# Optimization experiments

Hardware: AMD Instinct MI355X
Metric: run time of the kernel (lower is better)

## Reference

```python
import math
import jax, jax.numpy as jnp
import numpy as np

N = 50000          # nodes
E = 1_600_000      # edges
DNE = 128
DED = 128
NUM_RBF = 50
R_CUT = 5.0
LN_EPS = 1e-5


def setup_inputs() -> dict:
    key = jax.random.key(0)
    ks = jax.random.split(key, 16)
    z = jax.random.normal(ks[0], (N, 25), jnp.float32)
    edge = jax.random.randint(ks[1], (E, 2), 0, N, dtype=jnp.int64)
    r = jax.random.uniform(ks[2], (E,), jnp.float32) * (R_CUT * 1.1)  # some beyond cutoff
    u_raw = jax.random.normal(ks[3], (E, 3), jnp.float32)
    u = u_raw / jnp.linalg.norm(u_raw, axis=-1, keepdims=True)

    def xavier(k, shape):
        fan_in, fan_out = shape
        lim = math.sqrt(6.0 / (fan_in + fan_out))
        return jax.random.uniform(k, shape, jnp.float32, -lim, lim)

    return {
        "z": z, "edge": edge, "r": r, "u": u,
        "A_na_w": xavier(ks[4], (25, DNE)), "A_na_b": jnp.zeros((DNE,), jnp.float32),
        "A_nbr_w": xavier(ks[5], (25, DNE)), "A_nbr_b": jnp.zeros((DNE,), jnp.float32),
        "W_ndp_w": xavier(ks[6], (NUM_RBF, DNE)), "W_ndp_b": jnp.zeros((DNE,), jnp.float32),
        "W_nrd_w": xavier(ks[7], (2 * DNE, DNE)), "W_nrd_b": jnp.zeros((DNE,), jnp.float32),
        "W_nru_w": xavier(ks[8], (DNE, DNE)), "W_nru_b": jnp.zeros((DNE,), jnp.float32),
        "W_erp_w": xavier(ks[9], (NUM_RBF, DED)), "W_erp_b": jnp.zeros((DED,), jnp.float32),
        "ln_g": jnp.ones((DNE,), jnp.float32), "ln_b": jnp.zeros((DNE,), jnp.float32),
    }


def _sh_l2(u):
    x, y, zc = u[:, 0], u[:, 1], u[:, 2]
    s3 = math.sqrt(3.0)
    return jnp.stack([
        s3 * x * y,
        s3 * y * zc,
        0.5 * (3.0 * zc * zc - 1.0),
        s3 * zc * x,
        0.5 * s3 * (x * x - y * y),
    ], axis=-1)  # [E, 5]


def _rbf(r):
    start = math.exp(-R_CUT)
    means = jnp.linspace(start, 1.0, NUM_RBF)
    beta = (2.0 / NUM_RBF * (1.0 - start)) ** (-2)
    alpha = 5.0 / R_CUT
    return jnp.exp(-beta * (jnp.exp(-alpha * r[:, None]) - means) ** 2)  # [E, NUM_RBF]


def reference(z, edge, r, u,
              A_na_w, A_na_b, A_nbr_w, A_nbr_b,
              W_ndp_w, W_ndp_b, W_nrd_w, W_nrd_b,
              W_nru_w, W_nru_b, W_erp_w, W_erp_b,
              ln_g, ln_b):
    i, j = edge[:, 0], edge[:, 1]
    n_nodes = z.shape[0]

    # edge tensor representations (Lmax=2)
    rt0 = r[:, None]          # [E,1]
    rt1 = u                   # [E,3]
    rt2 = _sh_l2(u)           # [E,5]

    rbf = _rbf(r)                                              # [E,R]
    c = (0.5 * (jnp.cos(math.pi * r / R_CUT) + 1.0)
         * (r < R_CUT).astype(r.dtype))[:, None]               # [E,1]

    nbr = jax.nn.silu(z @ A_nbr_w + A_nbr_b)                   # [N,dne]
    gate = (rbf @ W_ndp_w + W_ndp_b) * c                       # [E,dne]
    msg = nbr[j] * gate                                        # gather + gate
    m = jax.ops.segment_sum(msg, i, num_segments=n_nodes)      # scatter-add [N,dne]

    na = jax.nn.silu(z @ A_na_w + A_na_b)
    h = jnp.concatenate([na, m], axis=-1) @ W_nrd_w + W_nrd_b  # [N,dne]
    mu = jnp.mean(h, axis=-1, keepdims=True)
    var = jnp.var(h, axis=-1, keepdims=True)
    h = (h - mu) / jnp.sqrt(var + LN_EPS) * ln_g + ln_b
    h = jax.nn.silu(h)
    h = h @ W_nru_w + W_nru_b                                  # [N,dne]

    t = (h[i] + h[j]) * (rbf @ W_erp_w + W_erp_b)              # [E,ded]
    return (h, t, rt0, rt1, rt2, c)
```

## Files before the change

kernel.cpp:

```cpp
#include <hip/hip_runtime.h>
#include <hip/hip_bf16.h>
#include <math.h>

#define NN 50000
#define NE 1600000
#define D 128
#define NRBF 50
#define RCUT 5.0f
#define LNEPS 1e-5f
#define EB 16
#define EB2 64
#define EDGE_GRID 2048
#define SCAN_B 196
#define NB 16
#define NPB 8

typedef __attribute__((ext_vector_type(8))) short bf16x8;
typedef __attribute__((ext_vector_type(4))) float f32x4;

__device__ __forceinline__ float silu_f(float x) {
    return x / (1.0f + __expf(-x));
}
__device__ __forceinline__ unsigned short f2bf(float x) {
    __hip_bfloat16 b = __float2bfloat16(x);
    return *reinterpret_cast<unsigned short*>(&b);
}
__device__ __forceinline__ float bf2f(unsigned short u) {
    unsigned int x = ((unsigned int)u) << 16;
    return __uint_as_float(x);
}

__global__ __launch_bounds__(128) void nbr_kernel(
    const float* __restrict__ z, const float* __restrict__ Aw,
    const float* __restrict__ Ab, unsigned short* __restrict__ nbr_bf)
{
    const int n = blockIdx.x;
    const int d = threadIdx.x;
    float acc = Ab[d];
#pragma unroll
    for (int k = 0; k < 25; ++k)
        acc = fmaf(z[n * 25 + k], Aw[k * D + d], acc);
    nbr_bf[(size_t)n * D + d] = f2bf(silu_f(acc));
}

__global__ __launch_bounds__(256) void aux_kernel(
    const int* __restrict__ edge, const float* __restrict__ r,
    const float* __restrict__ u, float* __restrict__ rt0,
    float* __restrict__ rt1, float* __restrict__ rt2,
    float* __restrict__ cout, int* __restrict__ cnt)
{
    const int e = blockIdx.x * 256 + threadIdx.x;
    if (e >= NE) return;
    const float rr = r[e];
    rt0[e] = rr;
    const float cc = (rr < RCUT)
        ? 0.5f * (__cosf(3.14159265358979f * rr * (1.0f / RCUT)) + 1.0f)
        : 0.0f;
    cout[e] = cc;
    const float x  = u[e * 3 + 0];
    const float y  = u[e * 3 + 1];
    const float zc = u[e * 3 + 2];
    rt1[(size_t)e * 3 + 0] = x;
    rt1[(size_t)e * 3 + 1] = y;
    rt1[(size_t)e * 3 + 2] = zc;
    const float s3 = 1.7320508075688772f;
    rt2[(size_t)e * 5 + 0] = s3 * x * y;
    rt2[(size_t)e * 5 + 1] = s3 * y * zc;
    rt2[(size_t)e * 5 + 2] = 0.5f * (3.0f * zc * zc - 1.0f);
    rt2[(size_t)e * 5 + 3] = s3 * zc * x;
    rt2[(size_t)e * 5 + 4] = 0.5f * s3 * (x * x - y * y);
    atomicAdd(&cnt[edge[2 * e]], 1);
}

__global__ __launch_bounds__(256) void scan1_kernel(
    const int* __restrict__ cnt, int* __restrict__ off, int* __restrict__ bsum)
{
    __shared__ int s[2][256];
    const int t = threadIdx.x;
    const int g = blockIdx.x * 256 + t;
    const int v = (g < NN) ? cnt[g] : 0;
    int incl = v;
    s[0][t] = incl;
    __syncthreads();
    int cur = 0;
#pragma unroll
    for (int dd = 1; dd < 256; dd <<= 1) {
        const int add = (t >= dd) ? s[cur][t - dd] : 0;
        incl += add;
        s[cur ^ 1][t] = incl;
        __syncthreads();
        cur ^= 1;
    }
    if (g < NN) off[g] = incl - v;
    if (t == 255) bsum[blockIdx.x] = incl;
}

__global__ __launch_bounds__(256) void scan2_kernel(int* __restrict__ bsum)
{
    __shared__ int s[2][256];
    const int t = threadIdx.x;
    const int v = (t < SCAN_B) ? bsum[t] : 0;
    int incl = v;
    s[0][t] = incl;
    __syncthreads();
    int cur = 0;
#pragma unroll
    for (int dd = 1; dd < 256; dd <<= 1) {
        const int add = (t >= dd) ? s[cur][t - dd] : 0;
        incl += add;
        s[cur ^ 1][t] = incl;
        __syncthreads();
        cur ^= 1;
    }
    if (t < SCAN_B) bsum[t] = incl - v;
}

__global__ __launch_bounds__(256) void scan3_kernel(
    int* __restrict__ off, const int* __restrict__ bsum)
{
    const int g = blockIdx.x * 256 + threadIdx.x;
    if (g < NN) off[g] += bsum[blockIdx.x];
    if (g == 0) off[NN] = NE;
}

__global__ __launch_bounds__(256) void scatter_kernel(
    const int* __restrict__ edge, const float* __restrict__ r,
    const int* __restrict__ off, int* __restrict__ cursor,
    uint2* __restrict__ jr)
{
    const int e = blockIdx.x * 256 + threadIdx.x;
    if (e >= NE) return;
    const int2 ep = ((const int2*)edge)[e];
    const int pos = atomicAdd(&cursor[ep.x], 1);
    uint2 v;
    v.x = (unsigned int)ep.y;
    v.y = __float_as_uint(r[e]);
    jr[off[ep.x] + pos] = v;
}

__global__ __launch_bounds__(128) void gather_msg_mfma(
    const uint2* __restrict__ jr, const int* __restrict__ off,
    const float* __restrict__ W_ndp, const float* __restrict__ b_ndp,
    const unsigned short* __restrict__ nbr_bf, float* __restrict__ m)
{
    __shared__ unsigned short P[EB][64];
    __shared__ float er_s[EB];
    __shared__ float c_s[EB];
    __shared__ int   j_s[EB];

    const int tid = threadIdx.x;
    const int w   = tid >> 6;
    const int l   = tid & 63;
    const int lr  = l & 15;
    const int lg  = l >> 4;

    bf16x8 wf[4][2];
#pragma unroll
    for (int dt = 0; dt < 4; ++dt) {
        const int col = w * 64 + lr * 4 + dt;
#pragma unroll
        for (int s = 0; s < 2; ++s) {
            bf16x8 v;
#pragma unroll
            for (int j = 0; j < 8; ++j) {
                const int k = s * 32 + lg * 8 + j;
                float wv = 0.0f;
                if (k < NRBF)       wv = W_ndp[k * D + col];
                else if (k == NRBF) wv = b_ndp[col];
                v[j] = (short)f2bf(wv);
            }
            wf[dt][s] = v;
        }
    }

    const float start = expf(-RCUT);
    const float step  = (1.0f - start) / (NRBF - 1);
    const float bq    = (2.0f / NRBF) * (1.0f - start);
    const float beta  = 1.0f / (bq * bq);

    const int prow = tid >> 3;
    const int pci  = tid & 7;

    for (int nn = 0; nn < NPB; ++nn) {
        const int n   = blockIdx.x * NPB + nn;
        const int s0  = off[n];
        const int deg = off[n + 1] - s0;

        f32x4 macc[4] = {{0,0,0,0},{0,0,0,0},{0,0,0,0},{0,0,0,0}};

        for (int base = 0; base < deg; base += EB) {
            const int chunk = min(EB, deg - base);
            if (tid < EB) {
                if (tid < chunk) {
                    const uint2 v = jr[s0 + base + tid];
                    const float rr = __uint_as_float(v.y);
                    er_s[tid] = __expf(-rr);
                    c_s[tid] = (rr < RCUT)
                        ? 0.5f * (__cosf(3.14159265358979f * rr * (1.0f / RCUT)) + 1.0f)
                        : 0.0f;
                    j_s[tid] = (int)v.x;
                } else {
                    er_s[tid] = 0.0f; c_s[tid] = 0.0f; j_s[tid] = 0;
                }
            }
            __syncthreads();
            {
                const float er = er_s[prow];
                const float cc = c_s[prow];
                unsigned int pk[4];
#pragma unroll
                for (int p2 = 0; p2 < 4; ++p2) {
                    unsigned int word = 0;
#pragma unroll
                    for (int c = 0; c < 2; ++c) {
                        const int k = pci * 8 + p2 * 2 + c;
                        float v = 0.0f;
                        if (k < NRBF) {
                            const float diff = er - (start + (float)k * step);
                            v = cc * __expf(-beta * diff * diff);
                        } else if (k == NRBF) {
                            v = cc;
                        }
                        word |= ((unsigned int)f2bf(v)) << (16 * c);
                    }
                    pk[p2] = word;
                }
                const int swc = pci ^ (prow & 7);
                *(uint4*)&P[prow][swc * 8] = make_uint4(pk[0], pk[1], pk[2], pk[3]);
            }
            __syncthreads();
            bf16x8 af[2];
#pragma unroll
            for (int s = 0; s < 2; ++s) {
                const int swc = (s * 4 + lg) ^ (lr & 7);
                af[s] = *(const bf16x8*)&P[lr][swc * 8];
            }
            f32x4 accs[4];
#pragma unroll
            for (int dt = 0; dt < 4; ++dt) {
                f32x4 acc = {0.0f, 0.0f, 0.0f, 0.0f};
                acc = __builtin_amdgcn_mfma_f32_16x16x32_bf16(af[0], wf[dt][0], acc, 0, 0, 0);
                acc = __builtin_amdgcn_mfma_f32_16x16x32_bf16(af[1], wf[dt][1], acc, 0, 0, 0);
                accs[dt] = acc;
            }
#pragma unroll
            for (int q = 0; q < 4; ++q) {
                const int row = j_s[lg * 4 + q];
                const uint2 nv8 = *(const uint2*)(nbr_bf + (size_t)row * D + w * 64 + lr * 4);
                const float n0 = bf2f((unsigned short)(nv8.x & 0xffff));
                const float n1 = bf2f((unsigned short)(nv8.x >> 16));
                const float n2 = bf2f((unsigned short)(nv8.y & 0xffff));
                const float n3 = bf2f((unsigned short)(nv8.y >> 16));
                macc[0][q] = fmaf(n0, accs[0][q], macc[0][q]);
                macc[1][q] = fmaf(n1, accs[1][q], macc[1][q]);
                macc[2][q] = fmaf(n2, accs[2][q], macc[2][q]);
                macc[3][q] = fmaf(n3, accs[3][q], macc[3][q]);
            }
            __syncthreads();
        }

        float v0 = macc[0][0] + macc[0][1] + macc[0][2] + macc[0][3];
        float v1 = macc[1][0] + macc[1][1] + macc[1][2] + macc[1][3];
        float v2 = macc[2][0] + macc[2][1] + macc[2][2] + macc[2][3];
        float v3 = macc[3][0] + macc[3][1] + macc[3][2] + macc[3][3];
        v0 += __shfl_xor(v0, 16); v0 += __shfl_xor(v0, 32);
        v1 += __shfl_xor(v1, 16); v1 += __shfl_xor(v1, 32);
        v2 += __shfl_xor(v2, 16); v2 += __shfl_xor(v2, 32);
        v3 += __shfl_xor(v3, 16); v3 += __shfl_xor(v3, 32);
        if (lg == 0) {
            float4 o = {v0, v1, v2, v3};
            *(float4*)&m[(size_t)n * D + w * 64 + lr * 4] = o;
        }
    }
}

__global__ __launch_bounds__(256) void node_kernel2(
    const float* __restrict__ z, const float* __restrict__ A_na_w,
    const float* __restrict__ A_na_b, const float* __restrict__ m,
    const float* __restrict__ W_nrd_w, const float* __restrict__ W_nrd_b,
    const float* __restrict__ W_nru_w, const float* __restrict__ W_nru_b,
    const float* __restrict__ ln_g, const float* __restrict__ ln_b,
    float* __restrict__ hout, unsigned short* __restrict__ h_bf)
{
    __shared__ float inbuf[NB][260];
    __shared__ float wbuf[32][128];
    __shared__ float part[4][NB][2];

    const int tid = threadIdx.x;
    const int n0 = blockIdx.x * NB;
    const int nl = tid & 15;
    const int dg = tid >> 4;

    for (int idx = tid; idx < NB * 128; idx += 256) {
        const int n = idx >> 7;
        const int d = idx & 127;
        float acc = A_na_b[d];
#pragma unroll
        for (int k = 0; k < 25; ++k)
            acc = fmaf(z[(size_t)(n0 + n) * 25 + k], A_na_w[k * D + d], acc);
        inbuf[n][d]       = silu_f(acc);
        inbuf[n][128 + d] = m[(size_t)(n0 + n) * D + d];
    }

    float h1[8];
#pragma unroll
    for (int dd = 0; dd < 8; ++dd) h1[dd] = W_nrd_b[dg * 8 + dd];

    for (int tile = 0; tile < 8; ++tile) {
        __syncthreads();
        for (int v = tid; v < 32 * 32; v += 256) {
            const int row = v >> 5;
            const int c4  = (v & 31) * 4;
            *(float4*)&wbuf[row][c4] =
                *(const float4*)&W_nrd_w[(size_t)(tile * 32 + row) * D + c4];
        }
        __syncthreads();
#pragma unroll 4
        for (int k = 0; k < 32; ++k) {
            const float rin = inbuf[nl][tile * 32 + k];
            const float4 wa = *(const float4*)&wbuf[k][dg * 8];
            const float4 wb = *(const float4*)&wbuf[k][dg * 8 + 4];
            h1[0] = fmaf(rin, wa.x, h1[0]);
            h1[1] = fmaf(rin, wa.y, h1[1]);
            h1[2] = fmaf(rin, wa.z, h1[2]);
            h1[3] = fmaf(rin, wa.w, h1[3]);
            h1[4] = fmaf(rin, wb.x, h1[4]);
            h1[5] = fmaf(rin, wb.y, h1[5]);
            h1[6] = fmaf(rin, wb.z, h1[6]);
            h1[7] = fmaf(rin, wb.w, h1[7]);
        }
    }

    float s = 0.0f, sq = 0.0f;
#pragma unroll
    for (int dd = 0; dd < 8; ++dd) { s += h1[dd]; sq += h1[dd] * h1[dd]; }
    s  += __shfl_xor(s, 16);  sq += __shfl_xor(sq, 16);
    s  += __shfl_xor(s, 32);  sq += __shfl_xor(sq, 32);
    const int wv = tid >> 6;
    if ((tid & 63) < 16) { part[wv][nl][0] = s; part[wv][nl][1] = sq; }
    __syncthreads();
    float ts = 0.0f, tsq = 0.0f;
#pragma unroll
    for (int w = 0; w < 4; ++w) { ts += part[w][nl][0]; tsq += part[w][nl][1]; }
    const float mu  = ts * (1.0f / 128.0f);
    const float var = tsq * (1.0f / 128.0f) - mu * mu;
    const float inv = rsqrtf(var + LNEPS);

#pragma unroll
    for (int dd = 0; dd < 8; ++dd) {
        const int d = dg * 8 + dd;
        inbuf[nl][d] = silu_f((h1[dd] - mu) * inv * ln_g[d] + ln_b[d]);
    }

    float h2[8];
#pragma unroll
    for (int dd = 0; dd < 8; ++dd) h2[dd] = W_nru_b[dg * 8 + dd];

    for (int tile = 0; tile < 4; ++tile) {
        __syncthreads();
        for (int v = tid; v < 32 * 32; v += 256) {
            const int row = v >> 5;
            const int c4  = (v & 31) * 4;
            *(float4*)&wbuf[row][c4] =
                *(const float4*)&W_nru_w[(size_t)(tile * 32 + row) * D + c4];
        }
        __syncthreads();
#pragma unroll 4
        for (int k = 0; k < 32; ++k) {
            const float rin = inbuf[nl][tile * 32 + k];
            const float4 wa = *(const float4*)&wbuf[k][dg * 8];
            const float4 wb = *(const float4*)&wbuf[k][dg * 8 + 4];
            h2[0] = fmaf(rin, wa.x, h2[0]);
            h2[1] = fmaf(rin, wa.y, h2[1]);
            h2[2] = fmaf(rin, wa.z, h2[2]);
            h2[3] = fmaf(rin, wa.w, h2[3]);
            h2[4] = fmaf(rin, wb.x, h2[4]);
            h2[5] = fmaf(rin, wb.y, h2[5]);
            h2[6] = fmaf(rin, wb.z, h2[6]);
            h2[7] = fmaf(rin, wb.w, h2[7]);
        }
    }

    float4 o0 = {h2[0], h2[1], h2[2], h2[3]};
    float4 o1 = {h2[4], h2[5], h2[6], h2[7]};
    *(float4*)&hout[(size_t)(n0 + nl) * D + dg * 8]     = o0;
    *(float4*)&hout[(size_t)(n0 + nl) * D + dg * 8 + 4] = o1;

    unsigned int b0 = (unsigned int)f2bf(h2[0]) | ((unsigned int)f2bf(h2[1]) << 16);
    unsigned int b1 = (unsigned int)f2bf(h2[2]) | ((unsigned int)f2bf(h2[3]) << 16);
    unsigned int b2 = (unsigned int)f2bf(h2[4]) | ((unsigned int)f2bf(h2[5]) << 16);
    unsigned int b3 = (unsigned int)f2bf(h2[6]) | ((unsigned int)f2bf(h2[7]) << 16);
    *(uint4*)&h_bf[(size_t)(n0 + nl) * D + dg * 8] = make_uint4(b0, b1, b2, b3);
}

__global__ __launch_bounds__(256) void edge_out_mfma(
    const int* __restrict__ edge, const float* __restrict__ r,
    const float* __restrict__ W_erp, const float* __restrict__ b_erp,
    const unsigned short* __restrict__ h_bf, float* __restrict__ t)
{
    __shared__ unsigned short P[EB2][64];
    __shared__ unsigned short hv[EB2][136];
    __shared__ int ij_s[EB2][2];

    const int tid = threadIdx.x;
    const int w  = tid >> 6;
    const int l  = tid & 63;
    const int lr = l & 15;
    const int lg = l >> 4;

    bf16x8 wf[8][2];
    float bias[8];
#pragma unroll
    for (int dt = 0; dt < 8; ++dt) {
        const int col = lr * 8 + dt;
        bias[dt] = b_erp[col];
#pragma unroll
        for (int s = 0; s < 2; ++s) {
            bf16x8 v;
#pragma unroll
            for (int j = 0; j < 8; ++j) {
                const int k = s * 32 + lg * 8 + j;
                v[j] = (k < NRBF) ? (short)f2bf(W_erp[k * D + col]) : (short)0;
            }
            wf[dt][s] = v;
        }
    }

    const float start = expf(-RCUT);
    const float step  = (1.0f - start) / (NRBF - 1);
    const float bq    = (2.0f / NRBF) * (1.0f - start);
    const float beta  = 1.0f / (bq * bq);

    const int prow  = tid & 63;
    const int kbase = (tid >> 6) * 16;

    const int nbatch = NE / EB2;
    for (int batch = blockIdx.x; batch < nbatch; batch += gridDim.x) {
        const int eb = batch * EB2;
        if (tid < EB2) {
            const int2 ep = ((const int2*)edge)[eb + tid];
            ij_s[tid][0] = ep.x;
            ij_s[tid][1] = ep.y;
        }
        {
            const float er = __expf(-r[eb + prow]);
            const int kc0 = kbase >> 3;
#pragma unroll
            for (int c2 = 0; c2 < 2; ++c2) {
                const int kc = kc0 + c2;
                unsigned int pk[4];
#pragma unroll
                for (int p2 = 0; p2 < 4; ++p2) {
                    unsigned int word = 0;
#pragma unroll
                    for (int c = 0; c < 2; ++c) {
                        const int k = kc * 8 + p2 * 2 + c;
                        float v = 0.0f;
                        if (k < NRBF) {
                            const float diff = er - (start + (float)k * step);
                            v = __expf(-beta * diff * diff);
                        }
                        word |= ((unsigned int)f2bf(v)) << (16 * c);
                    }
                    pk[p2] = word;
                }
                const int swc = kc ^ (prow & 7);
                *(uint4*)&P[prow][swc * 8] = make_uint4(pk[0], pk[1], pk[2], pk[3]);
            }
        }
        __syncthreads();

        const int arow = w * 16 + lr;
        bf16x8 af[2];
#pragma unroll
        for (int s = 0; s < 2; ++s) {
            const int swc = (s * 4 + lg) ^ (arow & 7);
            af[s] = *(const bf16x8*)&P[arow][swc * 8];
        }

#pragma unroll
        for (int idx = tid; idx < EB2 * 16; idx += 256) {
            const int el = idx >> 4;
            const int ch = idx & 15;
            const uint4 ui = *((const uint4*)(h_bf + (size_t)ij_s[el][0] * D) + ch);
            const uint4 uj = *((const uint4*)(h_bf + (size_t)ij_s[el][1] * D) + ch);
            const unsigned int wi[4] = {ui.x, ui.y, ui.z, ui.w};
            const unsigned int wj[4] = {uj.x, uj.y, uj.z, uj.w};
            unsigned int wo[4];
#pragma unroll
            for (int p = 0; p < 4; ++p) {
                const float lo = bf2f((unsigned short)(wi[p] & 0xffff))
                               + bf2f((unsigned short)(wj[p] & 0xffff));
                const float hi = bf2f((unsigned short)(wi[p] >> 16))
                               + bf2f((unsigned short)(wj[p] >> 16));
                wo[p] = (unsigned int)f2bf(lo) | ((unsigned int)f2bf(hi) << 16);
            }
            *(uint4*)&hv[el][ch * 8] = make_uint4(wo[0], wo[1], wo[2], wo[3]);
        }
        __syncthreads();

        f32x4 accs[8];
#pragma unroll
        for (int dt = 0; dt < 8; ++dt) {
            f32x4 acc = {0.0f, 0.0f, 0.0f, 0.0f};
            acc = __builtin_amdgcn_mfma_f32_16x16x32_bf16(af[0], wf[dt][0], acc, 0, 0, 0);
            acc = __builtin_amdgcn_mfma_f32_16x16x32_bf16(af[1], wf[dt][1], acc, 0, 0, 0);
            accs[dt] = acc;
        }
#pragma unroll
        for (int q = 0; q < 4; ++q) {
            const int el = w * 16 + lg * 4 + q;
            const bf16x8 hv8 = *(const bf16x8*)&hv[el][lr * 8];
            float o[8];
#pragma unroll
            for (int dt = 0; dt < 8; ++dt)
                o[dt] = bf2f((unsigned short)hv8[dt]) * (accs[dt][q] + bias[dt]);
            float4 o0 = {o[0], o[1], o[2], o[3]};
            float4 o1 = {o[4], o[5], o[6], o[7]};
            float* tp = &t[(size_t)(eb + el) * D + lr * 8];
            *(float4*)tp       = o0;
            *(float4*)(tp + 4) = o1;
        }
        __syncthreads();
    }
}

extern "C" void kernel_launch(void* const* d_in, const int* in_sizes, int n_in,
                              void* d_out, int out_size, void* d_ws, size_t ws_size,
                              hipStream_t stream) {
    const float* z      = (const float*)d_in[0];
    const int*   edge   = (const int*)d_in[1];
    const float* r      = (const float*)d_in[2];
    const float* u      = (const float*)d_in[3];
    const float* A_na_w  = (const float*)d_in[4];
    const float* A_na_b  = (const float*)d_in[5];
    const float* A_nbr_w = (const float*)d_in[6];
    const float* A_nbr_b = (const float*)d_in[7];
    const float* W_ndp_w = (const float*)d_in[8];
    const float* W_ndp_b = (const float*)d_in[9];
    const float* W_nrd_w = (const float*)d_in[10];
    const float* W_nrd_b = (const float*)d_in[11];
    const float* W_nru_w = (const float*)d_in[12];
    const float* W_nru_b = (const float*)d_in[13];
    const float* W_erp_w = (const float*)d_in[14];
    const float* W_erp_b = (const float*)d_in[15];
    const float* ln_g    = (const float*)d_in[16];
    const float* ln_b    = (const float*)d_in[17];

    float* out = (float*)d_out;
    float* h_out   = out;
    float* t_out   = out + (size_t)NN * D;
    float* rt0_out = t_out + (size_t)NE * D;
    float* rt1_out = rt0_out + (size_t)NE;
    float* rt2_out = rt1_out + (size_t)NE * 3;
    float* c_out   = rt2_out + (size_t)NE * 5;

    unsigned short* nbr_bf = (unsigned short*)d_ws;
    float* m_ws   = (float*)((char*)d_ws + (size_t)NN * D * sizeof(unsigned short));
    unsigned short* h_bf = (unsigned short*)((char*)m_ws + (size_t)NN * D * sizeof(float));

    uint2* jr   = (uint2*)t_out;
    int* off    = (int*)(jr + NE);
    int* cursor = off + (NN + 1);
    int* bsum   = cursor + NN;

    hipMemsetAsync(cursor, 0, (size_t)NN * sizeof(int), stream);

    nbr_kernel<<<NN, 128, 0, stream>>>(z, A_nbr_w, A_nbr_b, nbr_bf);

    aux_kernel<<<(NE + 255) / 256, 256, 0, stream>>>(
        edge, r, u, rt0_out, rt1_out, rt2_out, c_out, cursor);

    scan1_kernel<<<SCAN_B, 256, 0, stream>>>(cursor, off, bsum);
    scan2_kernel<<<1, 256, 0, stream>>>(bsum);
    scan3_kernel<<<SCAN_B, 256, 0, stream>>>(off, bsum);

    hipMemsetAsync(cursor, 0, (size_t)NN * sizeof(int), stream);

    scatter_kernel<<<(NE + 255) / 256, 256, 0, stream>>>(edge, r, off, cursor, jr);

    gather_msg_mfma<<<NN / NPB, 128, 0, stream>>>(
        jr, off, W_ndp_w, W_ndp_b, nbr_bf, m_ws);

    node_kernel2<<<NN / NB, 256, 0, stream>>>(
        z, A_na_w, A_na_b, m_ws, W_nrd_w, W_nrd_b,
        W_nru_w, W_nru_b, ln_g, ln_b, h_out, h_bf);

    edge_out_mfma<<<EDGE_GRID, 256, 0, stream>>>(
        edge, r, W_erp_w, W_erp_b, h_bf, t_out);
}
```

Baseline: 846.0 us.

## Process edges in CSR-sorted order in edge_out and defer aux outputs

Extends the CSR slot records to carry the original edge id and source node, then iterates edge_out_mfma over sorted slots so the h[i] gathers hit the same node row repeatedly, improving cache locality. The t writes become scattered by original edge id. The slot buffer moves into the rt2 output region, so the aux kernel that writes rt0/rt1/rt2/c runs last, and edge counting is split into its own kernel. Each edge's slot record grows from 8 to 16 bytes, and the cost of scattered float writes to t is traded for more local gathers.

```diff
diff --git a/kernel.cpp b/kernel.cpp
--- a/kernel.cpp
+++ b/kernel.cpp
@@ -43,11 +43,479 @@
     nbr_bf[(size_t)n * D + d] = f2bf(silu_f(acc));
 }
 
+__global__ __launch_bounds__(256) void count_kernel(
+    const int* __restrict__ edge, int* __restrict__ cnt)
+{
+    const int e = blockIdx.x * 256 + threadIdx.x;
+    if (e >= NE) return;
+    atomicAdd(&cnt[edge[2 * e]], 1);
+}
+
+__global__ __launch_bounds__(256) void scan1_kernel(
+    const int* __restrict__ cnt, int* __restrict__ off, int* __restrict__ bsum)
+{
+    __shared__ int s[2][256];
+    const int t = threadIdx.x;
+    const int g = blockIdx.x * 256 + t;
+    const int v = (g < NN) ? cnt[g] : 0;
+    int incl = v;
+    s[0][t] = incl;
+    __syncthreads();
+    int cur = 0;
+#pragma unroll
+    for (int dd = 1; dd < 256; dd <<= 1) {
+        const int add = (t >= dd) ? s[cur][t - dd] : 0;
+        incl += add;
+        s[cur ^ 1][t] = incl;
+        __syncthreads();
+        cur ^= 1;
+    }
+    if (g < NN) off[g] = incl - v;
+    if (t == 255) bsum[blockIdx.x] = incl;
+}
+
+__global__ __launch_bounds__(256) void scan2_kernel(int* __restrict__ bsum)
+{
+    __shared__ int s[2][256];
+    const int t = threadIdx.x;
+    const int v = (t < SCAN_B) ? bsum[t] : 0;
+    int incl = v;
+    s[0][t] = incl;
+    __syncthreads();
+    int cur = 0;
+#pragma unroll
+    for (int dd = 1; dd < 256; dd <<= 1) {
+        const int add = (t >= dd) ? s[cur][t - dd] : 0;
+        incl += add;
+        s[cur ^ 1][t] = incl;
+        __syncthreads();
+        cur ^= 1;
+    }
+    if (t < SCAN_B) bsum[t] = incl - v;
+}
+
+__global__ __launch_bounds__(256) void scan3_kernel(
+    int* __restrict__ off, const int* __restrict__ bsum)
+{
+    const int g = blockIdx.x * 256 + threadIdx.x;
+    if (g < NN) off[g] += bsum[blockIdx.x];
+    if (g == 0) off[NN] = NE;
+}
+
+__global__ __launch_bounds__(256) void scatter_kernel(
+    const int* __restrict__ edge, const float* __restrict__ r,
+    const int* __restrict__ off, int* __restrict__ cursor,
+    uint4* __restrict__ slots)
+{
+    const int e = blockIdx.x * 256 + threadIdx.x;
+    if (e >= NE) return;
+    const int2 ep = ((const int2*)edge)[e];
+    const int pos = atomicAdd(&cursor[ep.x], 1);
+    slots[off[ep.x] + pos] =
+        make_uint4((unsigned int)ep.y, __float_as_uint(r[e]),
+                   (unsigned int)e, (unsigned int)ep.x);
+}
+
+__global__ __launch_bounds__(128) void gather_msg_mfma(
+    const uint4* __restrict__ slots, const int* __restrict__ off,
+    const float* __restrict__ W_ndp, const float* __restrict__ b_ndp,
+    const unsigned short* __restrict__ nbr_bf, float* __restrict__ m)
+{
+    __shared__ unsigned short P[EB][64];
+    __shared__ float er_s[EB];
+    __shared__ float c_s[EB];
+    __shared__ int   j_s[EB];
+
+    const int tid = threadIdx.x;
+    const int w   = tid >> 6;
+    const int l   = tid & 63;
+    const int lr  = l & 15;
+    const int lg  = l >> 4;
+
+    bf16x8 wf[4][2];
+#pragma unroll
+    for (int dt = 0; dt < 4; ++dt) {
+        const int col = w * 64 + lr * 4 + dt;
+#pragma unroll
+        for (int s = 0; s < 2; ++s) {
+            bf16x8 v;
+#pragma unroll
+            for (int j = 0; j < 8; ++j) {
+                const int k = s * 32 + lg * 8 + j;
+                float wv = 0.0f;
+                if (k < NRBF)       wv = W_ndp[k * D + col];
+                else if (k == NRBF) wv = b_ndp[col];
+                v[j] = (short)f2bf(wv);
+            }
+            wf[dt][s] = v;
+        }
+    }
+
+    const float start = expf(-RCUT);
+    const float step  = (1.0f - start) / (NRBF - 1);
+    const float bq    = (2.0f / NRBF) * (1.0f - start);
+    const float beta  = 1.0f / (bq * bq);
+
+    const int prow = tid >> 3;
+    const int pci  = tid & 7;
+
+    for (int nn = 0; nn < NPB; ++nn) {
+        const int n   = blockIdx.x * NPB + nn;
+        const int s0  = off[n];
+        const int deg = off[n + 1] - s0;
+
+        f32x4 macc[4] = {{0,0,0,0},{0,0,0,0},{0,0,0,0},{0,0,0,0}};
+
+        for (int base = 0; base < deg; base += EB) {
+            const int chunk = min(EB, deg - base);
+            if (tid < EB) {
+                if (tid < chunk) {
+                    const uint4 v = slots[s0 + base + tid];
+                    const float rr = __uint_as_float(v.y);
+                    er_s[tid] = __expf(-rr);
+                    c_s[tid] = (rr < RCUT)
+                        ? 0.5f * (__cosf(3.14159265358979f * rr * (1.0f / RCUT)) + 1.0f)
+                        : 0.0f;
+                    j_s[tid] = (int)v.x;
+                } else {
+                    er_s[tid] = 0.0f; c_s[tid] = 0.0f; j_s[tid] = 0;
+                }
+            }
+            __syncthreads();
+            {
+                const float er = er_s[prow];
+                const float cc = c_s[prow];
+                unsigned int pk[4];
+#pragma unroll
+                for (int p2 = 0; p2 < 4; ++p2) {
+                    unsigned int word = 0;
+#pragma unroll
+                    for (int c = 0; c < 2; ++c) {
+                        const int k = pci * 8 + p2 * 2 + c;
+                        float v = 0.0f;
+                        if (k < NRBF) {
+                            const float diff = er - (start + (float)k * step);
+                            v = cc * __expf(-beta * diff * diff);
+                        } else if (k == NRBF) {
+                            v = cc;
+                        }
+                        word |= ((unsigned int)f2bf(v)) << (16 * c);
+                    }
+                    pk[p2] = word;
+                }
+                const int swc = pci ^ (prow & 7);
+                *(uint4*)&P[prow][swc * 8] = make_uint4(pk[0], pk[1], pk[2], pk[3]);
+            }
+            __syncthreads();
+            bf16x8 af[2];
+#pragma unroll
+            for (int s = 0; s < 2; ++s) {
+                const int swc = (s * 4 + lg) ^ (lr & 7);
+                af[s] = *(const bf16x8*)&P[lr][swc * 8];
+            }
+            f32x4 accs[4];
+#pragma unroll
+            for (int dt = 0; dt < 4; ++dt) {
+                f32x4 acc = {0.0f, 0.0f, 0.0f, 0.0f};
+                acc = __builtin_amdgcn_mfma_f32_16x16x32_bf16(af[0], wf[dt][0], acc, 0, 0, 0);
+                acc = __builtin_amdgcn_mfma_f32_16x16x32_bf16(af[1], wf[dt][1], acc, 0, 0, 0);
+                accs[dt] = acc;
+            }
+#pragma unroll
+            for (int q = 0; q < 4; ++q) {
+                const int row = j_s[lg * 4 + q];
+                const uint2 nv8 = *(const uint2*)(nbr_bf + (size_t)row * D + w * 64 + lr * 4);
+                const float n0 = bf2f((unsigned short)(nv8.x & 0xffff));
+                const float n1 = bf2f((unsigned short)(nv8.x >> 16));
+                const float n2 = bf2f((unsigned short)(nv8.y & 0xffff));
+                const float n3 = bf2f((unsigned short)(nv8.y >> 16));
+                macc[0][q] = fmaf(n0, accs[0][q], macc[0][q]);
+                macc[1][q] = fmaf(n1, accs[1][q], macc[1][q]);
+                macc[2][q] = fmaf(n2, accs[2][q], macc[2][q]);
+                macc[3][q] = fmaf(n3, accs[3][q], macc[3][q]);
+            }
+            __syncthreads();
+        }
+
+        float v0 = macc[0][0] + macc[0][1] + macc[0][2] + macc[0][3];
+        float v1 = macc[1][0] + macc[1][1] + macc[1][2] + macc[1][3];
+        float v2 = macc[2][0] + macc[2][1] + macc[2][2] + macc[2][3];
+        float v3 = macc[3][0] + macc[3][1] + macc[3][2] + macc[3][3];
+        v0 += __shfl_xor(v0, 16); v0 += __shfl_xor(v0, 32);
+        v1 += __shfl_xor(v1, 16); v1 += __shfl_xor(v1, 32);
+        v2 += __shfl_xor(v2, 16); v2 += __shfl_xor(v2, 32);
+        v3 += __shfl_xor(v3, 16); v3 += __shfl_xor(v3, 32);
+        if (lg == 0) {
+            float4 o = {v0, v1, v2, v3};
+            *(float4*)&m[(size_t)n * D + w * 64 + lr * 4] = o;
+        }
+    }
+}
+
+__global__ __launch_bounds__(256) void node_kernel2(
+    const float* __restrict__ z, const float* __restrict__ A_na_w,
+    const float* __restrict__ A_na_b, const float* __restrict__ m,
+    const float* __restrict__ W_nrd_w, const float* __restrict__ W_nrd_b,
+    const float* __restrict__ W_nru_w, const float* __restrict__ W_nru_b,
+    const float* __restrict__ ln_g, const float* __restrict__ ln_b,
+    float* __restrict__ hout, unsigned short* __restrict__ h_bf)
+{
+    __shared__ float inbuf[NB][260];
+    __shared__ float wbuf[32][128];
+    __shared__ float part[4][NB][2];
+
+    const int tid = threadIdx.x;
+    const int n0 = blockIdx.x * NB;
+    const int nl = tid & 15;
+    const int dg = tid >> 4;
+
+    for (int idx = tid; idx < NB * 128; idx += 256) {
+        const int n = idx >> 7;
+        const int d = idx & 127;
+        float acc = A_na_b[d];
+#pragma unroll
+        for (int k = 0; k < 25; ++k)
+            acc = fmaf(z[(size_t)(n0 + n) * 25 + k], A_na_w[k * D + d], acc);
+        inbuf[n][d]       = silu_f(acc);
+        inbuf[n][128 + d] = m[(size_t)(n0 + n) * D + d];
+    }
+
+    float h1[8];
+#pragma unroll
+    for (int dd = 0; dd < 8; ++dd) h1[dd] = W_nrd_b[dg * 8 + dd];
+
+    for (int tile = 0; tile < 8; ++tile) {
+        __syncthreads();
+        for (int v = tid; v < 32 * 32; v += 256) {
+            const int row = v >> 5;
+            const int c4  = (v & 31) * 4;
+            *(float4*)&wbuf[row][c4] =
+                *(const float4*)&W_nrd_w[(size_t)(tile * 32 + row) * D + c4];
+        }
+        __syncthreads();
+#pragma unroll 4
+        for (int k = 0; k < 32; ++k) {
+            const float rin = inbuf[nl][tile * 32 + k];
+            const float4 wa = *(const float4*)&wbuf[k][dg * 8];
+            const float4 wb = *(const float4*)&wbuf[k][dg * 8 + 4];
+            h1[0] = fmaf(rin, wa.x, h1[0]);
+            h1[1] = fmaf(rin, wa.y, h1[1]);
+            h1[2] = fmaf(rin, wa.z, h1[2]);
+            h1[3] = fmaf(rin, wa.w, h1[3]);
+            h1[4] = fmaf(rin, wb.x, h1[4]);
+            h1[5] = fmaf(rin, wb.y, h1[5]);
+            h1[6] = fmaf(rin, wb.z, h1[6]);
+            h1[7] = fmaf(rin, wb.w, h1[7]);
+        }
+    }
+
+    float s = 0.0f, sq = 0.0f;
+#pragma unroll
+    for (int dd = 0; dd < 8; ++dd) { s += h1[dd]; sq += h1[dd] * h1[dd]; }
+    s  += __shfl_xor(s, 16);  sq += __shfl_xor(sq, 16);
+    s  += __shfl_xor(s, 32);  sq += __shfl_xor(sq, 32);
+    const int wv = tid >> 6;
+    if ((tid & 63) < 16) { part[wv][nl][0] = s; part[wv][nl][1] = sq; }
+    __syncthreads();
+    float ts = 0.0f, tsq = 0.0f;
+#pragma unroll
+    for (int w = 0; w < 4; ++w) { ts += part[w][nl][0]; tsq += part[w][nl][1]; }
+    const float mu  = ts * (1.0f / 128.0f);
+    const float var = tsq * (1.0f / 128.0f) - mu * mu;
+    const float inv = rsqrtf(var + LNEPS);
+
+#pragma unroll
+    for (int dd = 0; dd < 8; ++dd) {
+        const int d = dg * 8 + dd;
+        inbuf[nl][d] = silu_f((h1[dd] - mu) * inv * ln_g[d] + ln_b[d]);
+    }
+
+    float h2[8];
+#pragma unroll
+    for (int dd = 0; dd < 8; ++dd) h2[dd] = W_nru_b[dg * 8 + dd];
+
+    for (int tile = 0; tile < 4; ++tile) {
+        __syncthreads();
+        for (int v = tid; v < 32 * 32; v += 256) {
+            const int row = v >> 5;
+            const int c4  = (v & 31) * 4;
+            *(float4*)&wbuf[row][c4] =
+                *(const float4*)&W_nru_w[(size_t)(tile * 32 + row) * D + c4];
+        }
+        __syncthreads();
+#pragma unroll 4
+        for (int k = 0; k < 32; ++k) {
+            const float rin = inbuf[nl][tile * 32 + k];
+            const float4 wa = *(const float4*)&wbuf[k][dg * 8];
+            const float4 wb = *(const float4*)&wbuf[k][dg * 8 + 4];
+            h2[0] = fmaf(rin, wa.x, h2[0]);
+            h2[1] = fmaf(rin, wa.y, h2[1]);
+            h2[2] = fmaf(rin, wa.z, h2[2]);
+            h2[3] = fmaf(rin, wa.w, h2[3]);
+            h2[4] = fmaf(rin, wb.x, h2[4]);
+            h2[5] = fmaf(rin, wb.y, h2[5]);
+            h2[6] = fmaf(rin, wb.z, h2[6]);
+            h2[7] = fmaf(rin, wb.w, h2[7]);
+        }
+    }
+
+    float4 o0 = {h2[0], h2[1], h2[2], h2[3]};
+    float4 o1 = {h2[4], h2[5], h2[6], h2[7]};
+    *(float4*)&hout[(size_t)(n0 + nl) * D + dg * 8]     = o0;
+    *(float4*)&hout[(size_t)(n0 + nl) * D + dg * 8 + 4] = o1;
+
+    unsigned int b0 = (unsigned int)f2bf(h2[0]) | ((unsigned int)f2bf(h2[1]) << 16);
+    unsigned int b1 = (unsigned int)f2bf(h2[2]) | ((unsigned int)f2bf(h2[3]) << 16);
+    unsigned int b2 = (unsigned int)f2bf(h2[4]) | ((unsigned int)f2bf(h2[5]) << 16);
+    unsigned int b3 = (unsigned int)f2bf(h2[6]) | ((unsigned int)f2bf(h2[7]) << 16);
+    *(uint4*)&h_bf[(size_t)(n0 + nl) * D + dg * 8] = make_uint4(b0, b1, b2, b3);
+}
+
+__global__ __launch_bounds__(256) void edge_out_mfma(
+    const uint4* __restrict__ slots, const float* __restrict__ W_erp,
+    const float* __restrict__ b_erp, const unsigned short* __restrict__ h_bf,
+    float* __restrict__ t)
+{
+    __shared__ unsigned short P[EB2][64];
+    __shared__ unsigned short hv[EB2][136];
+    __shared__ int ij_s[EB2][2];
+    __shared__ int e_s[EB2];
+    __shared__ float er_s[EB2];
+
+    const int tid = threadIdx.x;
+    const int w  = tid >> 6;
+    const int l  = tid & 63;
+    const int lr = l & 15;
+    const int lg = l >> 4;
+
+    bf16x8 wf[8][2];
+    float bias[8];
+#pragma unroll
+    for (int dt = 0; dt < 8; ++dt) {
+        const int col = lr * 8 + dt;
+        bias[dt] = b_erp[col];
+#pragma unroll
+        for (int s = 0; s < 2; ++s) {
+            bf16x8 v;
+#pragma unroll
+            for (int j = 0; j < 8; ++j) {
+                const int k = s * 32 + lg * 8 + j;
+                v[j] = (k < NRBF) ? (short)f2bf(W_erp[k * D + col]) : (short)0;
+            }
+            wf[dt][s] = v;
+        }
+    }
+
+    const float start = expf(-RCUT);
+    const float step  = (1.0f - start) / (NRBF - 1);
+    const float bq    = (2.0f / NRBF) * (1.0f - start);
+    const float beta  = 1.0f / (bq * bq);
+
+    const int prow  = tid & 63;
+    const int kbase = (tid >> 6) * 16;
+
+    const int nchunk = NE / EB2;
+    const int cpb = (nchunk + gridDim.x - 1) / gridDim.x;
+    const int cbeg = blockIdx.x * cpb;
+    const int cend = min(cbeg + cpb, nchunk);
+
+    for (int chunk = cbeg; chunk < cend; ++chunk) {
+        const int sb = chunk * EB2;
+        if (tid < EB2) {
+            const uint4 sv = slots[sb + tid];
+            ij_s[tid][1] = (int)sv.x;
+            er_s[tid]    = __expf(-__uint_as_float(sv.y));
+            e_s[tid]     = (int)sv.z;
+            ij_s[tid][0] = (int)sv.w;
+        }
+        __syncthreads();
+        {
+            const float er = er_s[prow];
+            const int kc0 = kbase >> 3;
+#pragma unroll
+            for (int c2 = 0; c2 < 2; ++c2) {
+                const int kc = kc0 + c2;
+                unsigned int pk[4];
+#pragma unroll
+                for (int p2 = 0; p2 < 4; ++p2) {
+                    unsigned int word = 0;
+#pragma unroll
+                    for (int c = 0; c < 2; ++c) {
+                        const int k = kc * 8 + p2 * 2 + c;
+                        float v = 0.0f;
+                        if (k < NRBF) {
+                            const float diff = er - (start + (float)k * step);
+                            v = __expf(-beta * diff * diff);
+                        }
+                        word |= ((unsigned int)f2bf(v)) << (16 * c);
+                    }
+                    pk[p2] = word;
+                }
+                const int swc = kc ^ (prow & 7);
+                *(uint4*)&P[prow][swc * 8] = make_uint4(pk[0], pk[1], pk[2], pk[3]);
+            }
+        }
+        __syncthreads();
+
+        const int arow = w * 16 + lr;
+        bf16x8 af[2];
+#pragma unroll
+        for (int s = 0; s < 2; ++s) {
+            const int swc = (s * 4 + lg) ^ (arow & 7);
+            af[s] = *(const bf16x8*)&P[arow][swc * 8];
+        }
+
+#pragma unroll
+        for (int idx = tid; idx < EB2 * 16; idx += 256) {
+            const int el = idx >> 4;
+            const int ch = idx & 15;
+            const uint4 ui = *((const uint4*)(h_bf + (size_t)ij_s[el][0] * D) + ch);
+            const uint4 uj = *((const uint4*)(h_bf + (size_t)ij_s[el][1] * D) + ch);
+            const unsigned int wi[4] = {ui.x, ui.y, ui.z, ui.w};
+            const unsigned int wj[4] = {uj.x, uj.y, uj.z, uj.w};
+            unsigned int wo[4];
+#pragma unroll
+            for (int p = 0; p < 4; ++p) {
+                const float lo = bf2f((unsigned short)(wi[p] & 0xffff))
+                               + bf2f((unsigned short)(wj[p] & 0xffff));
+                const float hi = bf2f((unsigned short)(wi[p] >> 16))
+                               + bf2f((unsigned short)(wj[p] >> 16));
+                wo[p] = (unsigned int)f2bf(lo) | ((unsigned int)f2bf(hi) << 16);
+            }
+            *(uint4*)&hv[el][ch * 8] = make_uint4(wo[0], wo[1], wo[2], wo[3]);
+        }
+        __syncthreads();
+
+        f32x4 accs[8];
+#pragma unroll
+        for (int dt = 0; dt < 8; ++dt) {
+            f32x4 acc = {0.0f, 0.0f, 0.0f, 0.0f};
+            acc = __builtin_amdgcn_mfma_f32_16x16x32_bf16(af[0], wf[dt][0], acc, 0, 0, 0);
+            acc = __builtin_amdgcn_mfma_f32_16x16x32_bf16(af[1], wf[dt][1], acc, 0, 0, 0);
+            accs[dt] = acc;
+        }
+#pragma unroll
+        for (int q = 0; q < 4; ++q) {
+            const int el = w * 16 + lg * 4 + q;
+            const bf16x8 hv8 = *(const bf16x8*)&hv[el][lr * 8];
+            float o[8];
+#pragma unroll
+            for (int dt = 0; dt < 8; ++dt)
+                o[dt] = bf2f((unsigned short)hv8[dt]) * (accs[dt][q] + bias[dt]);
+            float4 o0 = {o[0], o[1], o[2], o[3]};
+            float4 o1 = {o[4], o[5], o[6], o[7]};
+            float* tp = &t[(size_t)e_s[el] * D + lr * 8];
+            *(float4*)tp       = o0;
+            *(float4*)(tp + 4) = o1;
+        }
+        __syncthreads();
+    }
+}
+
 __global__ __launch_bounds__(256) void aux_kernel(
-    const int* __restrict__ edge, const float* __restrict__ r,
-    const float* __restrict__ u, float* __restrict__ rt0,
-    float* __restrict__ rt1, float* __restrict__ rt2,
-    float* __restrict__ cout, int* __restrict__ cnt)
+    const float* __restrict__ r, const float* __restrict__ u,
+    float* __restrict__ rt0, float* __restrict__ rt1,
+    float* __restrict__ rt2, float* __restrict__ cout)
 {
     const int e = blockIdx.x * 256 + threadIdx.x;
     if (e >= NE) return;
@@ -69,460 +537,6 @@
     rt2[(size_t)e * 5 + 2] = 0.5f * (3.0f * zc * zc - 1.0f);
     rt2[(size_t)e * 5 + 3] = s3 * zc * x;
     rt2[(size_t)e * 5 + 4] = 0.5f * s3 * (x * x - y * y);
-    atomicAdd(&cnt[edge[2 * e]], 1);
-}
-
-__global__ __launch_bounds__(256) void scan1_kernel(
-    const int* __restrict__ cnt, int* __restrict__ off, int* __restrict__ bsum)
-{
-    __shared__ int s[2][256];
-    const int t = threadIdx.x;
-    const int g = blockIdx.x * 256 + t;
-    const int v = (g < NN) ? cnt[g] : 0;
-    int incl = v;
-    s[0][t] = incl;
-    __syncthreads();
-    int cur = 0;
-#pragma unroll
-    for (int dd = 1; dd < 256; dd <<= 1) {
-        const int add = (t >= dd) ? s[cur][t - dd] : 0;
-        incl += add;
-        s[cur ^ 1][t] = incl;
-        __syncthreads();
-        cur ^= 1;
-    }
-    if (g < NN) off[g] = incl - v;
-    if (t == 255) bsum[blockIdx.x] = incl;
-}
-
-__global__ __launch_bounds__(256) void scan2_kernel(int* __restrict__ bsum)
-{
-    __shared__ int s[2][256];
-    const int t = threadIdx.x;
-    const int v = (t < SCAN_B) ? bsum[t] : 0;
-    int incl = v;
-    s[0][t] = incl;
-    __syncthreads();
-    int cur = 0;
-#pragma unroll
-    for (int dd = 1; dd < 256; dd <<= 1) {
-        const int add = (t >= dd) ? s[cur][t - dd] : 0;
-        incl += add;
-        s[cur ^ 1][t] = incl;
-        __syncthreads();
-        cur ^= 1;
-    }
-    if (t < SCAN_B) bsum[t] = incl - v;
-}
-
-__global__ __launch_bounds__(256) void scan3_kernel(
-    int* __restrict__ off, const int* __restrict__ bsum)
-{
-    const int g = blockIdx.x * 256 + threadIdx.x;
-    if (g < NN) off[g] += bsum[blockIdx.x];
-    if (g == 0) off[NN] = NE;
-}
-
-__global__ __launch_bounds__(256) void scatter_kernel(
-    const int* __restrict__ edge, const float* __restrict__ r,
-    const int* __restrict__ off, int* __restrict__ cursor,
-    uint2* __restrict__ jr)
-{
-    const int e = blockIdx.x * 256 + threadIdx.x;
-    if (e >= NE) return;
-    const int2 ep = ((const int2*)edge)[e];
-    const int pos = atomicAdd(&cursor[ep.x], 1);
-    uint2 v;
-    v.x = (unsigned int)ep.y;
-    v.y = __float_as_uint(r[e]);
-    jr[off[ep.x] + pos] = v;
-}
-
-__global__ __launch_bounds__(128) void gather_msg_mfma(
-    const uint2* __restrict__ jr, const int* __restrict__ off,
-    const float* __restrict__ W_ndp, const float* __restrict__ b_ndp,
-    const unsigned short* __restrict__ nbr_bf, float* __restrict__ m)
-{
-    __shared__ unsigned short P[EB][64];
-    __shared__ float er_s[EB];
-    __shared__ float c_s[EB];
-    __shared__ int   j_s[EB];
-
-    const int tid = threadIdx.x;
-    const int w   = tid >> 6;
-    const int l   = tid & 63;
-    const int lr  = l & 15;
-    const int lg  = l >> 4;
-
-    bf16x8 wf[4][2];
-#pragma unroll
-    for (int dt = 0; dt < 4; ++dt) {
-        const int col = w * 64 + lr * 4 + dt;
-#pragma unroll
-        for (int s = 0; s < 2; ++s) {
-            bf16x8 v;
-#pragma unroll
-            for (int j = 0; j < 8; ++j) {
-                const int k = s * 32 + lg * 8 + j;
-                float wv = 0.0f;
-                if (k < NRBF)       wv = W_ndp[k * D + col];
-                else if (k == NRBF) wv = b_ndp[col];
-                v[j] = (short)f2bf(wv);
-            }
-            wf[dt][s] = v;
-        }
-    }
-
-    const float start = expf(-RCUT);
-    const float step  = (1.0f - start) / (NRBF - 1);
-    const float bq    = (2.0f / NRBF) * (1.0f - start);
-    const float beta  = 1.0f / (bq * bq);
-
-    const int prow = tid >> 3;
-    const int pci  = tid & 7;
-
-    for (int nn = 0; nn < NPB; ++nn) {
-        const int n   = blockIdx.x * NPB + nn;
-        const int s0  = off[n];
-        const int deg = off[n + 1] - s0;
-
-        f32x4 macc[4] = {{0,0,0,0},{0,0,0,0},{0,0,0,0},{0,0,0,0}};
-
-        for (int base = 0; base < deg; base += EB) {
-            const int chunk = min(EB, deg - base);
-            if (tid < EB) {
-                if (tid < chunk) {
-                    const uint2 v = jr[s0 + base + tid];
-                    const float rr = __uint_as_float(v.y);
-                    er_s[tid] = __expf(-rr);
-                    c_s[tid] = (rr < RCUT)
-                        ? 0.5f * (__cosf(3.14159265358979f * rr * (1.0f / RCUT)) + 1.0f)
-                        : 0.0f;
-                    j_s[tid] = (int)v.x;
-                } else {
-                    er_s[tid] = 0.0f; c_s[tid] = 0.0f; j_s[tid] = 0;
-                }
-            }
-            __syncthreads();
-            {
-                const float er = er_s[prow];
-                const float cc = c_s[prow];
-                unsigned int pk[4];
-#pragma unroll
-                for (int p2 = 0; p2 < 4; ++p2) {
-                    unsigned int word = 0;
-#pragma unroll
-                    for (int c = 0; c < 2; ++c) {
-                        const int k = pci * 8 + p2 * 2 + c;
-                        float v = 0.0f;
-                        if (k < NRBF) {
-                            const float diff = er - (start + (float)k * step);
-                            v = cc * __expf(-beta * diff * diff);
-                        } else if (k == NRBF) {
-                            v = cc;
-                        }
-                        word |= ((unsigned int)f2bf(v)) << (16 * c);
-                    }
-                    pk[p2] = word;
-                }
-                const int swc = pci ^ (prow & 7);
-                *(uint4*)&P[prow][swc * 8] = make_uint4(pk[0], pk[1], pk[2], pk[3]);
-            }
-            __syncthreads();
-            bf16x8 af[2];
-#pragma unroll
-            for (int s = 0; s < 2; ++s) {
-                const int swc = (s * 4 + lg) ^ (lr & 7);
-                af[s] = *(const bf16x8*)&P[lr][swc * 8];
-            }
-            f32x4 accs[4];
-#pragma unroll
-            for (int dt = 0; dt < 4; ++dt) {
-                f32x4 acc = {0.0f, 0.0f, 0.0f, 0.0f};
-                acc = __builtin_amdgcn_mfma_f32_16x16x32_bf16(af[0], wf[dt][0], acc, 0, 0, 0);
-                acc = __builtin_amdgcn_mfma_f32_16x16x32_bf16(af[1], wf[dt][1], acc, 0, 0, 0);
-                accs[dt] = acc;
-            }
-#pragma unroll
-            for (int q = 0; q < 4; ++q) {
-                const int row = j_s[lg * 4 + q];
-                const uint2 nv8 = *(const uint2*)(nbr_bf + (size_t)row * D + w * 64 + lr * 4);
-                const float n0 = bf2f((unsigned short)(nv8.x & 0xffff));
-                const float n1 = bf2f((unsigned short)(nv8.x >> 16));
-                const float n2 = bf2f((unsigned short)(nv8.y & 0xffff));
-                const float n3 = bf2f((unsigned short)(nv8.y >> 16));
-                macc[0][q] = fmaf(n0, accs[0][q], macc[0][q]);
-                macc[1][q] = fmaf(n1, accs[1][q], macc[1][q]);
-                macc[2][q] = fmaf(n2, accs[2][q], macc[2][q]);
-                macc[3][q] = fmaf(n3, accs[3][q], macc[3][q]);
-            }
-            __syncthreads();
-        }
-
-        float v0 = macc[0][0] + macc[0][1] + macc[0][2] + macc[0][3];
-        float v1 = macc[1][0] + macc[1][1] + macc[1][2] + macc[1][3];
-        float v2 = macc[2][0] + macc[2][1] + macc[2][2] + macc[2][3];
-        float v3 = macc[3][0] + macc[3][1] + macc[3][2] + macc[3][3];
-        v0 += __shfl_xor(v0, 16); v0 += __shfl_xor(v0, 32);
-        v1 += __shfl_xor(v1, 16); v1 += __shfl_xor(v1, 32);
-        v2 += __shfl_xor(v2, 16); v2 += __shfl_xor(v2, 32);
-        v3 += __shfl_xor(v3, 16); v3 += __shfl_xor(v3, 32);
-        if (lg == 0) {
-            float4 o = {v0, v1, v2, v3};
-            *(float4*)&m[(size_t)n * D + w * 64 + lr * 4] = o;
-        }
-    }
-}
-
-__global__ __launch_bounds__(256) void node_kernel2(
-    const float* __restrict__ z, const float* __restrict__ A_na_w,
-    const float* __restrict__ A_na_b, const float* __restrict__ m,
-    const float* __restrict__ W_nrd_w, const float* __restrict__ W_nrd_b,
-    const float* __restrict__ W_nru_w, const float* __restrict__ W_nru_b,
-    const float* __restrict__ ln_g, const float* __restrict__ ln_b,
-    float* __restrict__ hout, unsigned short* __restrict__ h_bf)
-{
-    __shared__ float inbuf[NB][260];
-    __shared__ float wbuf[32][128];
-    __shared__ float part[4][NB][2];
-
-    const int tid = threadIdx.x;
-    const int n0 = blockIdx.x * NB;
-    const int nl = tid & 15;
-    const int dg = tid >> 4;
-
-    for (int idx = tid; idx < NB * 128; idx += 256) {
-        const int n = idx >> 7;
-        const int d = idx & 127;
-        float acc = A_na_b[d];
-#pragma unroll
-        for (int k = 0; k < 25; ++k)
-            acc = fmaf(z[(size_t)(n0 + n) * 25 + k], A_na_w[k * D + d], acc);
-        inbuf[n][d]       = silu_f(acc);
-        inbuf[n][128 + d] = m[(size_t)(n0 + n) * D + d];
-    }
-
-    float h1[8];
-#pragma unroll
-    for (int dd = 0; dd < 8; ++dd) h1[dd] = W_nrd_b[dg * 8 + dd];
-
-    for (int tile = 0; tile < 8; ++tile) {
-        __syncthreads();
-        for (int v = tid; v < 32 * 32; v += 256) {
-            const int row = v >> 5;
-            const int c4  = (v & 31) * 4;
-            *(float4*)&wbuf[row][c4] =
-                *(const float4*)&W_nrd_w[(size_t)(tile * 32 + row) * D + c4];
-        }
-        __syncthreads();
-#pragma unroll 4
-        for (int k = 0; k < 32; ++k) {
-            const float rin = inbuf[nl][tile * 32 + k];
-            const float4 wa = *(const float4*)&wbuf[k][dg * 8];
-            const float4 wb = *(const float4*)&wbuf[k][dg * 8 + 4];
-            h1[0] = fmaf(rin, wa.x, h1[0]);
-            h1[1] = fmaf(rin, wa.y, h1[1]);
-            h1[2] = fmaf(rin, wa.z, h1[2]);
-            h1[3] = fmaf(rin, wa.w, h1[3]);
-            h1[4] = fmaf(rin, wb.x, h1[4]);
-            h1[5] = fmaf(rin, wb.y, h1[5]);
-            h1[6] = fmaf(rin, wb.z, h1[6]);
-            h1[7] = fmaf(rin, wb.w, h1[7]);
-        }
-    }
-
-    float s = 0.0f, sq = 0.0f;
-#pragma unroll
-    for (int dd = 0; dd < 8; ++dd) { s += h1[dd]; sq += h1[dd] * h1[dd]; }
-    s  += __shfl_xor(s, 16);  sq += __shfl_xor(sq, 16);
-    s  += __shfl_xor(s, 32);  sq += __shfl_xor(sq, 32);
-    const int wv = tid >> 6;
-    if ((tid & 63) < 16) { part[wv][nl][0] = s; part[wv][nl][1] = sq; }
-    __syncthreads();
-    float ts = 0.0f, tsq = 0.0f;
-#pragma unroll
-    for (int w = 0; w < 4; ++w) { ts += part[w][nl][0]; tsq += part[w][nl][1]; }
-    const float mu  = ts * (1.0f / 128.0f);
-    const float var = tsq * (1.0f / 128.0f) - mu * mu;
-    const float inv = rsqrtf(var + LNEPS);
-
-#pragma unroll
-    for (int dd = 0; dd < 8; ++dd) {
-        const int d = dg * 8 + dd;
-        inbuf[nl][d] = silu_f((h1[dd] - mu) * inv * ln_g[d] + ln_b[d]);
-    }
-
-    float h2[8];
-#pragma unroll
-    for (int dd = 0; dd < 8; ++dd) h2[dd] = W_nru_b[dg * 8 + dd];
-
-    for (int tile = 0; tile < 4; ++tile) {
-        __syncthreads();
-        for (int v = tid; v < 32 * 32; v += 256) {
-            const int row = v >> 5;
-            const int c4  = (v & 31) * 4;
-            *(float4*)&wbuf[row][c4] =
-                *(const float4*)&W_nru_w[(size_t)(tile * 32 + row) * D + c4];
-        }
-        __syncthreads();
-#pragma unroll 4
-        for (int k = 0; k < 32; ++k) {
-            const float rin = inbuf[nl][tile * 32 + k];
-            const float4 wa = *(const float4*)&wbuf[k][dg * 8];
-            const float4 wb = *(const float4*)&wbuf[k][dg * 8 + 4];
-            h2[0] = fmaf(rin, wa.x, h2[0]);
-            h2[1] = fmaf(rin, wa.y, h2[1]);
-            h2[2] = fmaf(rin, wa.z, h2[2]);
-            h2[3] = fmaf(rin, wa.w, h2[3]);
-            h2[4] = fmaf(rin, wb.x, h2[4]);
-            h2[5] = fmaf(rin, wb.y, h2[5]);
-            h2[6] = fmaf(rin, wb.z, h2[6]);
-            h2[7] = fmaf(rin, wb.w, h2[7]);
-        }
-    }
-
-    float4 o0 = {h2[0], h2[1], h2[2], h2[3]};
-    float4 o1 = {h2[4], h2[5], h2[6], h2[7]};
-    *(float4*)&hout[(size_t)(n0 + nl) * D + dg * 8]     = o0;
-    *(float4*)&hout[(size_t)(n0 + nl) * D + dg * 8 + 4] = o1;
-
-    unsigned int b0 = (unsigned int)f2bf(h2[0]) | ((unsigned int)f2bf(h2[1]) << 16);
-    unsigned int b1 = (unsigned int)f2bf(h2[2]) | ((unsigned int)f2bf(h2[3]) << 16);
-    unsigned int b2 = (unsigned int)f2bf(h2[4]) | ((unsigned int)f2bf(h2[5]) << 16);
-    unsigned int b3 = (unsigned int)f2bf(h2[6]) | ((unsigned int)f2bf(h2[7]) << 16);
-    *(uint4*)&h_bf[(size_t)(n0 + nl) * D + dg * 8] = make_uint4(b0, b1, b2, b3);
-}
-
-__global__ __launch_bounds__(256) void edge_out_mfma(
-    const int* __restrict__ edge, const float* __restrict__ r,
-    const float* __restrict__ W_erp, const float* __restrict__ b_erp,
-    const unsigned short* __restrict__ h_bf, float* __restrict__ t)
-{
-    __shared__ unsigned short P[EB2][64];
-    __shared__ unsigned short hv[EB2][136];
-    __shared__ int ij_s[EB2][2];
-
-    const int tid = threadIdx.x;
-    const int w  = tid >> 6;
-    const int l  = tid & 63;
-    const int lr = l & 15;
-    const int lg = l >> 4;
-
-    bf16x8 wf[8][2];
-    float bias[8];
-#pragma unroll
-    for (int dt = 0; dt < 8; ++dt) {
-        const int col = lr * 8 + dt;
-        bias[dt] = b_erp[col];
-#pragma unroll
-        for (int s = 0; s < 2; ++s) {
-            bf16x8 v;
-#pragma unroll
-            for (int j = 0; j < 8; ++j) {
-                const int k = s * 32 + lg * 8 + j;
-                v[j] = (k < NRBF) ? (short)f2bf(W_erp[k * D + col]) : (short)0;
-            }
-            wf[dt][s] = v;
-        }
-    }
-
-    const float start = expf(-RCUT);
-    const float step  = (1.0f - start) / (NRBF - 1);
-    const float bq    = (2.0f / NRBF) * (1.0f - start);
-    const float beta  = 1.0f / (bq * bq);
-
-    const int prow  = tid & 63;
-    const int kbase = (tid >> 6) * 16;
-
-    const int nbatch = NE / EB2;
-    for (int batch = blockIdx.x; batch < nbatch; batch += gridDim.x) {
-        const int eb = batch * EB2;
-        if (tid < EB2) {
-            const int2 ep = ((const int2*)edge)[eb + tid];
-            ij_s[tid][0] = ep.x;
-            ij_s[tid][1] = ep.y;
-        }
-        {
-            const float er = __expf(-r[eb + prow]);
-            const int kc0 = kbase >> 3;
-#pragma unroll
-            for (int c2 = 0; c2 < 2; ++c2) {
-                const int kc = kc0 + c2;
-                unsigned int pk[4];
-#pragma unroll
-                for (int p2 = 0; p2 < 4; ++p2) {
-                    unsigned int word = 0;
-#pragma unroll
-                    for (int c = 0; c < 2; ++c) {
-                        const int k = kc * 8 + p2 * 2 + c;
-                        float v = 0.0f;
-                        if (k < NRBF) {
-                            const float diff = er - (start + (float)k * step);
-                            v = __expf(-beta * diff * diff);
-                        }
-                        word |= ((unsigned int)f2bf(v)) << (16 * c);
-                    }
-                    pk[p2] = word;
-                }
-                const int swc = kc ^ (prow & 7);
-                *(uint4*)&P[prow][swc * 8] = make_uint4(pk[0], pk[1], pk[2], pk[3]);
-            }
-        }
-        __syncthreads();
-
-        const int arow = w * 16 + lr;
-        bf16x8 af[2];
-#pragma unroll
-        for (int s = 0; s < 2; ++s) {
-            const int swc = (s * 4 + lg) ^ (arow & 7);
-            af[s] = *(const bf16x8*)&P[arow][swc * 8];
-        }
-
-#pragma unroll
-        for (int idx = tid; idx < EB2 * 16; idx += 256) {
-            const int el = idx >> 4;
-            const int ch = idx & 15;
-            const uint4 ui = *((const uint4*)(h_bf + (size_t)ij_s[el][0] * D) + ch);
-            const uint4 uj = *((const uint4*)(h_bf + (size_t)ij_s[el][1] * D) + ch);
-            const unsigned int wi[4] = {ui.x, ui.y, ui.z, ui.w};
-            const unsigned int wj[4] = {uj.x, uj.y, uj.z, uj.w};
-            unsigned int wo[4];
-#pragma unroll
-            for (int p = 0; p < 4; ++p) {
-                const float lo = bf2f((unsigned short)(wi[p] & 0xffff))
-                               + bf2f((unsigned short)(wj[p] & 0xffff));
-                const float hi = bf2f((unsigned short)(wi[p] >> 16))
-                               + bf2f((unsigned short)(wj[p] >> 16));
-                wo[p] = (unsigned int)f2bf(lo) | ((unsigned int)f2bf(hi) << 16);
-            }
-            *(uint4*)&hv[el][ch * 8] = make_uint4(wo[0], wo[1], wo[2], wo[3]);
-        }
-        __syncthreads();
-
-        f32x4 accs[8];
-#pragma unroll
-        for (int dt = 0; dt < 8; ++dt) {
-            f32x4 acc = {0.0f, 0.0f, 0.0f, 0.0f};
-            acc = __builtin_amdgcn_mfma_f32_16x16x32_bf16(af[0], wf[dt][0], acc, 0, 0, 0);
-            acc = __builtin_amdgcn_mfma_f32_16x16x32_bf16(af[1], wf[dt][1], acc, 0, 0, 0);
-            accs[dt] = acc;
-        }
-#pragma unroll
-        for (int q = 0; q < 4; ++q) {
-            const int el = w * 16 + lg * 4 + q;
-            const bf16x8 hv8 = *(const bf16x8*)&hv[el][lr * 8];
-            float o[8];
-#pragma unroll
-            for (int dt = 0; dt < 8; ++dt)
-                o[dt] = bf2f((unsigned short)hv8[dt]) * (accs[dt][q] + bias[dt]);
-            float4 o0 = {o[0], o[1], o[2], o[3]};
-            float4 o1 = {o[4], o[5], o[6], o[7]};
-            float* tp = &t[(size_t)(eb + el) * D + lr * 8];
-            *(float4*)tp       = o0;
-            *(float4*)(tp + 4) = o1;
-        }
-        __syncthreads();
-    }
 }
 
 extern "C" void kernel_launch(void* const* d_in, const int* in_sizes, int n_in,
@@ -559,17 +573,16 @@
     float* m_ws   = (float*)((char*)d_ws + (size_t)NN * D * sizeof(unsigned short));
     unsigned short* h_bf = (unsigned short*)((char*)m_ws + (size_t)NN * D * sizeof(float));
 
-    uint2* jr   = (uint2*)t_out;
-    int* off    = (int*)(jr + NE);
-    int* cursor = off + (NN + 1);
-    int* bsum   = cursor + NN;
+    uint4* slots = (uint4*)rt2_out;
+    int* off     = (int*)(slots + NE);
+    int* cursor  = off + (NN + 1);
+    int* bsum    = cursor + NN;
 
     hipMemsetAsync(cursor, 0, (size_t)NN * sizeof(int), stream);
 
     nbr_kernel<<<NN, 128, 0, stream>>>(z, A_nbr_w, A_nbr_b, nbr_bf);
 
-    aux_kernel<<<(NE + 255) / 256, 256, 0, stream>>>(
-        edge, r, u, rt0_out, rt1_out, rt2_out, c_out, cursor);
+    count_kernel<<<(NE + 255) / 256, 256, 0, stream>>>(edge, cursor);
 
     scan1_kernel<<<SCAN_B, 256, 0, stream>>>(cursor, off, bsum);
     scan2_kernel<<<1, 256, 0, stream>>>(bsum);
@@ -577,15 +590,18 @@
 
     hipMemsetAsync(cursor, 0, (size_t)NN * sizeof(int), stream);
 
-    scatter_kernel<<<(NE + 255) / 256, 256, 0, stream>>>(edge, r, off, cursor, jr);
+    scatter_kernel<<<(NE + 255) / 256, 256, 0, stream>>>(edge, r, off, cursor, slots);
 
     gather_msg_mfma<<<NN / NPB, 128, 0, stream>>>(
-        jr, off, W_ndp_w, W_ndp_b, nbr_bf, m_ws);
+        slots, off, W_ndp_w, W_ndp_b, nbr_bf, m_ws);
 
     node_kernel2<<<NN / NB, 256, 0, stream>>>(
         z, A_na_w, A_na_b, m_ws, W_nrd_w, W_nrd_b,
         W_nru_w, W_nru_b, ln_g, ln_b, h_out, h_bf);
 
     edge_out_mfma<<<EDGE_GRID, 256, 0, stream>>>(
-        edge, r, W_erp_w, W_erp_b, h_bf, t_out);
-}
+        slots, W_erp_w, W_erp_b, h_bf, t_out);
+
+    aux_kernel<<<(NE + 255) / 256, 256, 0, stream>>>(
+        r, u, rt0_out, rt1_out, rt2_out, c_out);
+}
```

After: 856.1 us. No clear change (+1.2%).
